# Performance work log

Measured on AMD Instinct MI355X. Metric: run time of the kernel, lower is better.

Reference implementation:

```python
import jax, jax.numpy as jnp
import numpy as np

NC = 256        # number of query contexts
N_ANS = 500000  # answer bank size
N_CTX = 500000  # context bank size
DIM = 128       # embedding dim
K = 32          # topk width


def setup_inputs() -> dict:
    key = jax.random.key(0)
    k1, k2, k3 = jax.random.split(key, 3)
    contexts = jax.random.normal(k1, (NC, DIM), dtype=jnp.float32)
    enc_ans = jax.random.normal(k2, (N_ANS, DIM), dtype=jnp.float32)
    enc_ctx = jax.random.normal(k3, (N_CTX, DIM), dtype=jnp.float32)
    return {"contexts": contexts, "enc_ans": enc_ans, "enc_ctx": enc_ctx, "k": K}


def reference(contexts, enc_ans, enc_ctx, k):
    # Hop 1: find k most similar contexts in the context bank.
    sims_ctx = jnp.einsum('qd,nd->qn', contexts, enc_ctx)          # [nc, N_ctx]
    _, c_ixs = jax.lax.top_k(sims_ctx, k)                          # [nc, k]
    # Gather neighbor contexts and average them (vectorized form of the
    # original per-row list comprehension + cat).
    new_contexts = enc_ctx[c_ixs].mean(axis=1)                     # [nc, dim]
    # Hop 2: rank answers against the averaged neighbor contexts.
    sims_ans = jnp.einsum('qd,nd->qn', new_contexts, enc_ans)      # [nc, N_ans]
    _, ixs = jax.lax.top_k(sims_ans, k)                            # [nc, k] int
    return ixs
```

## Files before the change

### kernel.cpp

```cpp
#include <hip/hip_runtime.h>
#include <hip/hip_bf16.h>
#include <float.h>


#define TILE 64
#define KSEL 32
#define TSEL 64
#define CB   128
#define LROW 136
#define NT_MAX 7936
#define EQCAP 256
#define POOLCAP 256

typedef __attribute__((ext_vector_type(8))) short s16x8;
typedef __attribute__((ext_vector_type(4))) float f32x4;

__device__ __forceinline__ unsigned f2key(float f) {
  unsigned u = __float_as_uint(f);
  return (u & 0x80000000u) ? ~u : (u | 0x80000000u);
}

__global__ void cvt_a_kernel(const float* __restrict__ A,
                             unsigned short* __restrict__ Abf, int nelem) {
  int i = blockIdx.x * 256 + threadIdx.x;
  if (i < nelem) Abf[i] = (unsigned short)(__float_as_uint(A[i]) >> 16);
}

__global__ __launch_bounds__(256) void score_mfma_kernel(
    const unsigned short* __restrict__ Abf,
    const float* __restrict__ bank,
    int n, int NT,
    float* __restrict__ tilemax) {
  __shared__ unsigned short bsm[CB * LROW];
  const int t = threadIdx.x;
  const int base = blockIdx.x * CB;

#pragma unroll
  for (int i = 0; i < 16; ++i) {
    int c = t + i * 256;
    int row = c >> 5;
    int c4  = c & 31;
    int g = base + row;
    float4 v = make_float4(0.f, 0.f, 0.f, 0.f);
    if (g < n) v = *(const float4*)(bank + (size_t)g * 128 + c4 * 4);
    unsigned int p0 = (__float_as_uint(v.y) & 0xffff0000u) | (__float_as_uint(v.x) >> 16);
    unsigned int p1 = (__float_as_uint(v.w) & 0xffff0000u) | (__float_as_uint(v.z) >> 16);
    *(uint2*)(bsm + row * LROW + c4 * 4) = make_uint2(p0, p1);
  }
  __syncthreads();

  const int wave = t >> 6;
  const int lane = t & 63;
  const int quad = lane >> 4;
  const int lh   = lane & 15;
  const int q0   = wave * 64;

  s16x8 afr[4][4];
#pragma unroll
  for (int qb = 0; qb < 4; ++qb)
#pragma unroll
    for (int k = 0; k < 4; ++k)
      afr[qb][k] = *(const s16x8*)(Abf + (size_t)(q0 + qb * 16 + lh) * 128 + k * 32 + quad * 8);

#pragma unroll
  for (int tl = 0; tl < 2; ++tl) {
    int tile_g = blockIdx.x * 2 + tl;
    f32x4 vmax[4];
#pragma unroll
    for (int qb = 0; qb < 4; ++qb) vmax[qb] = f32x4{-FLT_MAX, -FLT_MAX, -FLT_MAX, -FLT_MAX};

#pragma unroll
    for (int cb = 0; cb < 4; ++cb) {
      int crow = tl * 64 + cb * 16 + lh;
      s16x8 bfr[4];
#pragma unroll
      for (int k = 0; k < 4; ++k)
        bfr[k] = *(const s16x8*)(bsm + crow * LROW + k * 32 + quad * 8);
#pragma unroll
      for (int qb = 0; qb < 4; ++qb) {
        f32x4 acc = {0.f, 0.f, 0.f, 0.f};
#pragma unroll
        for (int k = 0; k < 4; ++k)
          acc = __builtin_amdgcn_mfma_f32_16x16x32_bf16(afr[qb][k], bfr[k], acc, 0, 0, 0);
#pragma unroll
        for (int r = 0; r < 4; ++r) vmax[qb][r] = fmaxf(vmax[qb][r], acc[r]);
      }
    }

    if (tile_g < NT) {
#pragma unroll
      for (int qb = 0; qb < 4; ++qb) {
#pragma unroll
        for (int r = 0; r < 4; ++r) {
          float v = vmax[qb][r];
          v = fmaxf(v, __shfl_xor(v, 1, 64));
          v = fmaxf(v, __shfl_xor(v, 2, 64));
          v = fmaxf(v, __shfl_xor(v, 4, 64));
          v = fmaxf(v, __shfl_xor(v, 8, 64));
          if (lh == 0)
            tilemax[(size_t)(q0 + qb * 16 + quad * 4 + r) * NT + tile_g] = v;
        }
      }
    }
  }
}

struct RadixSM {
  int hist[4][256];
  int ss[256];
  unsigned prefix;
  int t;
};

__device__ __forceinline__ void radix_select(const unsigned* __restrict__ key,
                                             int N, int target, int tid,
                                             RadixSM* sm,
                                             unsigned* outK, int* out_tres) {
  if (tid == 0) { sm->prefix = 0u; sm->t = target; }
  __syncthreads();
  const int wv = tid >> 6;
  for (int r = 0; r < 4; ++r) {
    const int shift = 24 - 8 * r;
    const unsigned kmask = (r == 0) ? 0u : (0xFFFFFFFFu << (32 - 8 * r));
    sm->hist[0][tid] = 0; sm->hist[1][tid] = 0;
    sm->hist[2][tid] = 0; sm->hist[3][tid] = 0;
    __syncthreads();
    const unsigned pref = sm->prefix;
    for (int i = tid; i < N; i += 256) {
      unsigned k = key[i];
      if ((k & kmask) == pref) atomicAdd(&sm->hist[wv][(k >> shift) & 255], 1);
    }
    __syncthreads();
    int v = sm->hist[0][tid] + sm->hist[1][tid] + sm->hist[2][tid] + sm->hist[3][tid];
    sm->ss[tid] = v;
    __syncthreads();
    for (int d = 1; d < 256; d <<= 1) {
      int add = (tid + d < 256) ? sm->ss[tid + d] : 0;
      __syncthreads();
      v += add;
      sm->ss[tid] = v;
      __syncthreads();
    }
    const int tcur = sm->t;
    const int hiCnt = (tid < 255) ? sm->ss[tid + 1] : 0;
    __syncthreads();
    if (v >= tcur && hiCnt < tcur) {
      sm->prefix = pref | ((unsigned)tid << shift);
      sm->t = tcur - hiCnt;
    }
    __syncthreads();
  }
  *outK = sm->prefix;
  *out_tres = sm->t;
}

__global__ __launch_bounds__(256) void select_tiles_kernel(
    const float* __restrict__ tilemax,
    int NT,
    int* __restrict__ sel_g) {
  const int q = blockIdx.x;
  const int t = threadIdx.x;
  __shared__ unsigned key[NT_MAX];
  __shared__ RadixSM rsm;
  __shared__ int n_hi, n_eq;
  __shared__ int eqs[EQCAP];

  if (t < TSEL) sel_g[(size_t)q * TSEL + t] = 0;

  for (int i = t; i < NT; i += 256)
    key[i] = f2key(tilemax[(size_t)q * NT + i]);
  if (t == 0) { n_hi = 0; n_eq = 0; }
  __syncthreads();

  unsigned K; int tres;
  radix_select(key, NT, TSEL, t, &rsm, &K, &tres);

  for (int i = t; i < NT; i += 256) {
    unsigned k = key[i];
    if (k > K) {
      int p = atomicAdd(&n_hi, 1);
      if (p < TSEL) sel_g[(size_t)q * TSEL + p] = i;
    } else if (k == K) {
      int p = atomicAdd(&n_eq, 1);
      if (p < EQCAP) eqs[p] = i;
    }
  }
  __syncthreads();
  const int nh = n_hi < TSEL ? n_hi : TSEL;
  const int ne = n_eq < EQCAP ? n_eq : EQCAP;
  if (t < ne) {
    int mine = eqs[t];
    int rank = 0;
    for (int j = 0; j < ne; ++j) rank += (eqs[j] < mine) ? 1 : 0;
    if (rank < tres && nh + rank < TSEL)
      sel_g[(size_t)q * TSEL + nh + rank] = mine;
  }
}

__global__ __launch_bounds__(256) void rescore_kernel(
    const float* __restrict__ A,
    const float* __restrict__ bank,
    int n,
    const int* __restrict__ sel_g,
    float* __restrict__ sc) {
  const int q = blockIdx.x >> 4;
  const int part = blockIdx.x & 15;
  const int t = threadIdx.x;
  __shared__ __align__(16) float aq[128];
  __shared__ int tiles[4];
  if (t < 128) aq[t] = A[(size_t)q * 128 + t];
  if (t >= 128 && t < 132)
    tiles[t - 128] = sel_g[(size_t)q * TSEL + part * 4 + (t - 128)];
  __syncthreads();

  const int tile = tiles[t >> 6];
  const int cand = tile * TILE + (t & 63);
  float s = -FLT_MAX;
  if (cand >= 0 && cand < n) {
    const float* row = bank + (size_t)cand * 128;
    float a0 = 0.f, a1 = 0.f;
#pragma unroll
    for (int i = 0; i < 128; i += 8) {
      float4 b0 = *(const float4*)(row + i);
      float4 b1 = *(const float4*)(row + i + 4);
      float4 x0 = *(const float4*)(aq + i);
      float4 x1 = *(const float4*)(aq + i + 4);
      a0 += x0.x * b0.x + x0.y * b0.y + x0.z * b0.z + x0.w * b0.w;
      a1 += x1.x * b1.x + x1.y * b1.y + x1.z * b1.z + x1.w * b1.w;
    }
    s = a0 + a1;
  }
  sc[(size_t)q * (TSEL * TILE) + part * 256 + t] = s;
}

__global__ __launch_bounds__(256) void topk_kernel(
    const int* __restrict__ sel_g,
    const float* __restrict__ sc,
    int* __restrict__ out) {
  const int q = blockIdx.x;
  const int t = threadIdx.x;
  __shared__ unsigned key[TSEL * TILE];
  __shared__ int sel_s[TSEL];
  __shared__ RadixSM rsm;
  __shared__ int n_pool;
  __shared__ int poolc[POOLCAP];
  __shared__ unsigned poolk[POOLCAP];

  if (t < TSEL) sel_s[t] = sel_g[(size_t)q * TSEL + t];
  for (int j = t; j < TSEL * TILE; j += 256)
    key[j] = f2key(sc[(size_t)q * (TSEL * TILE) + j]);
  if (t == 0) n_pool = 0;
  __syncthreads();

  unsigned K; int tres;
  radix_select(key, TSEL * TILE, KSEL, t, &rsm, &K, &tres);
  (void)tres;

  for (int j = t; j < TSEL * TILE; j += 256) {
    unsigned k = key[j];
    if (k >= K) {
      int p = atomicAdd(&n_pool, 1);
      if (p < POOLCAP) {
        poolk[p] = k;
        poolc[p] = sel_s[j >> 6] * TILE + (j & 63);
      }
    }
  }
  __syncthreads();
  const int np = n_pool < POOLCAP ? n_pool : POOLCAP;
  if (t < np) {
    unsigned mk = poolk[t];
    int mc = poolc[t];
    int rank = 0;
    for (int j = 0; j < np; ++j) {
      unsigned k = poolk[j];
      int c = poolc[j];
      rank += (k > mk || (k == mk && c < mc)) ? 1 : 0;
    }
    if (rank < KSEL) out[(size_t)q * KSEL + rank] = mc;
  }
}

__global__ void mean_gather_kernel(
    const float* __restrict__ bank,
    const int* __restrict__ ixs,
    float* __restrict__ outA,
    unsigned short* __restrict__ outAbf) {
  const int q = blockIdx.x;
  const int d = threadIdx.x;
  float s = 0.f;
  for (int j = 0; j < KSEL; ++j)
    s += bank[(size_t)ixs[q * KSEL + j] * 128 + d];
  s *= (1.0f / 32.0f);
  outA[(size_t)q * 128 + d] = s;
  outAbf[(size_t)q * 128 + d] = (unsigned short)(__float_as_uint(s) >> 16);
}

extern "C" void kernel_launch(void* const* d_in, const int* in_sizes, int n_in,
                              void* d_out, int out_size, void* d_ws, size_t ws_size,
                              hipStream_t stream) {
  const float* contexts = (const float*)d_in[0];
  const float* enc_ans  = (const float*)d_in[1];
  const float* enc_ctx  = (const float*)d_in[2];
  const int n_ans = in_sizes[1] / 128;
  const int n_ctx = in_sizes[2] / 128;
  const int NT_ctx = (n_ctx + TILE - 1) / TILE;
  const int NT_ans = (n_ans + TILE - 1) / TILE;
  const int NT_big = NT_ctx > NT_ans ? NT_ctx : NT_ans;
  const int NB_ctx = (n_ctx + CB - 1) / CB;
  const int NB_ans = (n_ans + CB - 1) / CB;

  char* ws = (char*)d_ws;
  size_t off = 0;
  float* tilemax = (float*)(ws + off);
  off += ((size_t)256 * NT_big * 4 + 255) & ~(size_t)255;
  int* c_ixs = (int*)(ws + off);
  off += ((size_t)256 * KSEL * 4 + 255) & ~(size_t)255;
  float* new_ctx = (float*)(ws + off);
  off += ((size_t)256 * 128 * 4 + 255) & ~(size_t)255;
  unsigned short* Abf1 = (unsigned short*)(ws + off);
  off += ((size_t)256 * 128 * 2 + 255) & ~(size_t)255;
  unsigned short* Abf2 = (unsigned short*)(ws + off);

  float* sc = tilemax;
  int* sel_g = (int*)Abf1;

  cvt_a_kernel<<<128, 256, 0, stream>>>(contexts, Abf1, 256 * 128);
  score_mfma_kernel<<<NB_ctx, 256, 0, stream>>>(Abf1, enc_ctx, n_ctx, NT_ctx, tilemax);
  select_tiles_kernel<<<256, 256, 0, stream>>>(tilemax, NT_ctx, sel_g);
  rescore_kernel<<<4096, 256, 0, stream>>>(contexts, enc_ctx, n_ctx, sel_g, sc);
  topk_kernel<<<256, 256, 0, stream>>>(sel_g, sc, c_ixs);
  mean_gather_kernel<<<256, 128, 0, stream>>>(enc_ctx, c_ixs, new_ctx, Abf2);

  score_mfma_kernel<<<NB_ans, 256, 0, stream>>>(Abf2, enc_ans, n_ans, NT_ans, tilemax);
  select_tiles_kernel<<<256, 256, 0, stream>>>(tilemax, NT_ans, sel_g);
  rescore_kernel<<<4096, 256, 0, stream>>>(new_ctx, enc_ans, n_ans, sel_g, sc);
  topk_kernel<<<256, 256, 0, stream>>>(sel_g, sc, (int*)d_out);
}
```

Measured before the change: 914.6 us.

## Load bank rows directly into MFMA fragments, bypassing shared-memory staging

```diff
diff --git a/kernel.cpp b/kernel.cpp
--- a/kernel.cpp
+++ b/kernel.cpp
@@ -7,7 +7,6 @@
 #define KSEL 32
 #define TSEL 64
 #define CB   128
-#define LROW 136
 #define NT_MAX 7936
 #define EQCAP 256
 #define POOLCAP 256
@@ -18,6 +17,15 @@
 __device__ __forceinline__ unsigned f2key(float f) {
   unsigned u = __float_as_uint(f);
   return (u & 0x80000000u) ? ~u : (u | 0x80000000u);
+}
+
+__device__ __forceinline__ s16x8 pack_bf16(float4 a, float4 b) {
+  union { s16x8 v; unsigned u[4]; } r;
+  r.u[0] = (__float_as_uint(a.y) & 0xffff0000u) | (__float_as_uint(a.x) >> 16);
+  r.u[1] = (__float_as_uint(a.w) & 0xffff0000u) | (__float_as_uint(a.z) >> 16);
+  r.u[2] = (__float_as_uint(b.y) & 0xffff0000u) | (__float_as_uint(b.x) >> 16);
+  r.u[3] = (__float_as_uint(b.w) & 0xffff0000u) | (__float_as_uint(b.z) >> 16);
+  return r.v;
 }
 
 __global__ void cvt_a_kernel(const float* __restrict__ A,
@@ -26,29 +34,13 @@
   if (i < nelem) Abf[i] = (unsigned short)(__float_as_uint(A[i]) >> 16);
 }
 
-__global__ __launch_bounds__(256) void score_mfma_kernel(
+__global__ __launch_bounds__(256, 3) void score_mfma_kernel(
     const unsigned short* __restrict__ Abf,
     const float* __restrict__ bank,
     int n, int NT,
     float* __restrict__ tilemax) {
-  __shared__ unsigned short bsm[CB * LROW];
   const int t = threadIdx.x;
   const int base = blockIdx.x * CB;
-
-#pragma unroll
-  for (int i = 0; i < 16; ++i) {
-    int c = t + i * 256;
-    int row = c >> 5;
-    int c4  = c & 31;
-    int g = base + row;
-    float4 v = make_float4(0.f, 0.f, 0.f, 0.f);
-    if (g < n) v = *(const float4*)(bank + (size_t)g * 128 + c4 * 4);
-    unsigned int p0 = (__float_as_uint(v.y) & 0xffff0000u) | (__float_as_uint(v.x) >> 16);
-    unsigned int p1 = (__float_as_uint(v.w) & 0xffff0000u) | (__float_as_uint(v.z) >> 16);
-    *(uint2*)(bsm + row * LROW + c4 * 4) = make_uint2(p0, p1);
-  }
-  __syncthreads();
-
   const int wave = t >> 6;
   const int lane = t & 63;
   const int quad = lane >> 4;
@@ -62,6 +54,8 @@
     for (int k = 0; k < 4; ++k)
       afr[qb][k] = *(const s16x8*)(Abf + (size_t)(q0 + qb * 16 + lh) * 128 + k * 32 + quad * 8);
 
+  const float4 z4 = make_float4(0.f, 0.f, 0.f, 0.f);
+
 #pragma unroll
   for (int tl = 0; tl < 2; ++tl) {
     int tile_g = blockIdx.x * 2 + tl;
@@ -71,11 +65,19 @@
 
 #pragma unroll
     for (int cb = 0; cb < 4; ++cb) {
-      int crow = tl * 64 + cb * 16 + lh;
+      int crow = base + tl * 64 + cb * 16 + lh;
+      bool ok = crow < n;
+      const float* rp = bank + (size_t)crow * 128 + quad * 8;
+      float4 fa[4], fb[4];
+#pragma unroll
+      for (int k = 0; k < 4; ++k) {
+        fa[k] = ok ? *(const float4*)(rp + k * 32)     : z4;
+        fb[k] = ok ? *(const float4*)(rp + k * 32 + 4) : z4;
+      }
       s16x8 bfr[4];
 #pragma unroll
-      for (int k = 0; k < 4; ++k)
-        bfr[k] = *(const s16x8*)(bsm + crow * LROW + k * 32 + quad * 8);
+      for (int k = 0; k < 4; ++k) bfr[k] = pack_bf16(fa[k], fb[k]);
+
 #pragma unroll
       for (int qb = 0; qb < 4; ++qb) {
         f32x4 acc = {0.f, 0.f, 0.f, 0.f};
```

Measured after the change: 1.880 ms. 106% more time.
